# Kernel tuning notes

Hardware: AMD Instinct MI355X
Metric: run time of the kernel (lower is better)

Reference implementation:

```python
import jax, jax.numpy as jnp
import numpy as np

DIM = 128
N_ROUNDS = 120


def _mlp(x, W1, b1, W2, b2, W3, b3):
    h = jax.nn.relu(x @ W1.T + b1)
    h = jax.nn.relu(h @ W2.T + b2)
    return h @ W3.T + b3


def _lstm(x, h, c, Wih, Whh, bih, bhh):
    # torch nn.LSTM gate order: i, f, g, o
    g = x @ Wih.T + h @ Whh.T + (bih + bhh)
    i, f, gg, o = jnp.split(g, 4, axis=-1)
    c2 = jax.nn.sigmoid(f) * c + jax.nn.sigmoid(i) * jnp.tanh(gg)
    h2 = jax.nn.sigmoid(o) * jnp.tanh(c2)
    return h2, c2


def setup_inputs() -> dict:
    key = jax.random.key(0)
    keys = iter(jax.random.split(key, 64))
    def w(*shape):
        return jax.random.normal(next(keys), shape, dtype=jnp.float32) * 0.05
    n_nodes, n_vars = 8000, 1000
    N = n_nodes + n_vars
    # sparse 0/1 adjacency, stored dense as in the original (adj_matrix.values)
    adj = (jax.random.uniform(next(keys), (n_nodes, N)) < 0.003).astype(jnp.float32)
    values = jax.random.randint(next(keys), (N,), 0, 2)
    inp = dict(adj=adj, values=values, n_nodes=n_nodes)
    inp.update(true_W=w(DIM, 1), true_b=w(DIM), false_W=w(DIM, 1), false_b=w(DIM))
    for p in ("cm", "pm"):
        inp.update({p + "_W1": w(DIM, DIM), p + "_b1": w(DIM),
                    p + "_W2": w(DIM, DIM), p + "_b2": w(DIM),
                    p + "_W3": w(DIM, DIM), p + "_b3": w(DIM)})
    inp.update(vv_W1=w(DIM, DIM), vv_b1=w(DIM), vv_W2=w(DIM, DIM), vv_b2=w(DIM),
               vv_W3=w(1, DIM), vv_b3=w(1))
    for p in ("vu", "nu"):
        inp.update({p + "_Wih": w(4 * DIM, DIM), p + "_Whh": w(4 * DIM, DIM),
                    p + "_bih": w(4 * DIM), p + "_bhh": w(4 * DIM)})
    return inp


def reference(adj, values, n_nodes, true_W, true_b, false_W, false_b,
              cm_W1, cm_b1, cm_W2, cm_b2, cm_W3, cm_b3,
              pm_W1, pm_b1, pm_W2, pm_b2, pm_W3, pm_b3,
              vv_W1, vv_b1, vv_W2, vv_b2, vv_W3, vv_b3,
              vu_Wih, vu_Whh, vu_bih, vu_bhh,
              nu_Wih, nu_Whh, nu_bih, nu_bhh):
    init_ts = jnp.ones((1,), jnp.float32)
    true_vec = true_W @ init_ts + true_b     # (128,)
    false_vec = false_W @ init_ts + false_b  # (128,)
    h0 = jnp.where((values == 1)[:, None], true_vec, false_vec)  # (N,128)
    c0 = jnp.zeros_like(h0)

    def step(carry, _):
        h, c = carry
        var_pre = _mlp(h, cm_W1, cm_b1, cm_W2, cm_b2, cm_W3, cm_b3)   # (N,128)
        c2p = adj @ var_pre                                           # (n_nodes,128)
        hn, cn = _lstm(c2p, h[:n_nodes], c[:n_nodes], vu_Wih, vu_Whh, vu_bih, vu_bhh)
        h = jnp.concatenate([hn, h[n_nodes:]], axis=0)
        c = jnp.concatenate([cn, c[n_nodes:]], axis=0)
        node_pre = _mlp(h[:n_nodes], pm_W1, pm_b1, pm_W2, pm_b2, pm_W3, pm_b3)
        p2c = adj.T @ node_pre                                        # (N,128)
        h, c = _lstm(p2c, h, c, nu_Wih, nu_Whh, nu_bih, nu_bhh)
        return (h, c), None

    (h, c), _ = jax.lax.scan(step, (h0, c0), None, length=N_ROUNDS)
    vote = _mlp(h[n_nodes:], vv_W1, vv_b1, vv_W2, vv_b2, vv_W3, vv_b3)  # (n_vars,1)
    return vote.squeeze(-1)
```

## Files before the change

### kernel.cpp

```cpp
#include <hip/hip_runtime.h>
#include <cstddef>
#include <cstdint>

#define DIM 128
#define NROUNDS 120
#define NNZ_CAP (1 << 20)
#define NB 250
#define IDXCAP 3584
#define RING 6

typedef _Float16 half8 __attribute__((ext_vector_type(8)));
typedef float f32x4 __attribute__((ext_vector_type(4)));
typedef unsigned long long u64;

__device__ __forceinline__ float sigf(float x) { return 1.f / (1.f + __expf(-x)); }
__device__ __forceinline__ float tanh_fast(float x) { return 2.f / (1.f + __expf(-2.f * x)) - 1.f; }

__device__ __forceinline__ void st_bypass(_Float16* p, _Float16 v) {
  union { _Float16 f; unsigned short s; } u;
  u.f = v;
  __hip_atomic_store((unsigned short*)p, u.s, __ATOMIC_RELAXED, __HIP_MEMORY_SCOPE_AGENT);
}

__global__ void count_nz_kernel(const float* __restrict__ adj, int* __restrict__ row_cnt,
                                int* __restrict__ col_cnt, int ncols) {
  int i = blockIdx.x;
  int t4 = blockIdx.y * blockDim.x + threadIdx.x;
  int j0 = t4 * 4;
  int c = 0;
  if (j0 < ncols) {
    if ((ncols & 3) == 0) {
      float4 v = *(const float4*)(adj + (size_t)i * ncols + j0);
      if (v.x != 0.f) { atomicAdd(&col_cnt[j0 + 0], 1); ++c; }
      if (v.y != 0.f) { atomicAdd(&col_cnt[j0 + 1], 1); ++c; }
      if (v.z != 0.f) { atomicAdd(&col_cnt[j0 + 2], 1); ++c; }
      if (v.w != 0.f) { atomicAdd(&col_cnt[j0 + 3], 1); ++c; }
    } else {
      for (int e = 0; e < 4 && j0 + e < ncols; ++e)
        if (adj[(size_t)i * ncols + j0 + e] != 0.f) { atomicAdd(&col_cnt[j0 + e], 1); ++c; }
    }
  }
  for (int off = 32; off; off >>= 1) c += __shfl_down(c, off, 64);
  if ((threadIdx.x & 63) == 0 && c) atomicAdd(&row_cnt[i], c);
}

__global__ void scan_kernel(const int* __restrict__ cnt, int* __restrict__ ptr, int n) {
  __shared__ int sdata[256];
  int t = threadIdx.x;
  int per = (n + 255) / 256;
  int beg = t * per;
  int end = beg + per; if (end > n) end = n;
  int local = 0;
  for (int i = beg; i < end; ++i) local += cnt[i];
  sdata[t] = local;
  __syncthreads();
  for (int off = 1; off < 256; off <<= 1) {
    int v = (t >= off) ? sdata[t - off] : 0;
    __syncthreads();
    sdata[t] += v;
    __syncthreads();
  }
  int run = sdata[t] - local;
  for (int i = beg; i < end; ++i) { ptr[i] = run; run += cnt[i]; }
  if (t == 255) ptr[n] = sdata[255];
}

__global__ void copy_int_kernel(const int* __restrict__ a, int* __restrict__ b, int n) {
  int i = blockIdx.x * 256 + threadIdx.x;
  if (i < n) b[i] = a[i];
}

__global__ __launch_bounds__(64) void fill_csr_csc_kernel(const float* __restrict__ adj,
                                                          const int* __restrict__ row_ptr,
                                                          int* __restrict__ col_idx,
                                                          int* __restrict__ col_cur,
                                                          int* __restrict__ row_idx, int ncols) {
  int row = blockIdx.x;
  int lane = threadIdx.x;
  int base = row_ptr[row];
  int cursor = 0;
  const float* arow = adj + (size_t)row * ncols;
  for (int j0 = 0; j0 < ncols; j0 += 64) {
    int j = j0 + lane;
    bool nz = (j < ncols) && (arow[j] != 0.f);
    u64 m = __ballot(nz);
    int pre = __popcll(m & ((1ull << lane) - 1));
    if (nz) {
      col_idx[base + cursor + pre] = j;
      int t = atomicAdd(&col_cur[j], 1);
      row_idx[t] = row;
    }
    cursor += __popcll(m);
  }
}

__global__ void pack_w_kernel(const float* __restrict__ src, int out_dim,
                              _Float16* __restrict__ dh) {
  int idx = blockIdx.x * 256 + threadIdx.x;
  if (idx >= out_dim * DIM) return;
  int n = idx >> 7, k = idx & 127;
  _Float16 hi = (_Float16)src[idx];
  int nt = n >> 4, ks = k >> 5;
  int L = ((k >> 3) & 3) * 16 + (n & 15);
  int j = k & 7;
  dh[((nt * 4 + ks) * 64 + L) * 8 + j] = hi;
}

__global__ void pack_bias_kernel(const float* __restrict__ a, const float* __restrict__ b,
                                 float* __restrict__ o, int n) {
  int i = blockIdx.x * 256 + threadIdx.x;
  if (i < n) o[i] = a[i] + b[i];
}

__device__ __forceinline__ int sw_idx(int m, int k) {
  return (m << 7) + (((((k >> 3) ^ (m & 15))) << 3) | (k & 7));
}

__device__ __forceinline__ float touch(const _Float16* __restrict__ w, int n, int tid) {
  float t = 0.f;
  for (int i = tid * 64; i < n; i += 512 * 64) t += (float)w[i];
  return t;
}

template <int NS>
__device__ __forceinline__ void gather_lds(const int* Sidx, const int* lofs, const int* lcnt,
                                           int mbase,
                                           const int* __restrict__ gptr,
                                           const int* __restrict__ gidx,
                                           const _Float16* __restrict__ va, int rowlim,
                                           int b, int nb, _Float16* Xh, _Float16* Xl, int tid) {
  int seg = tid & 15;
  const char* vab = (const char*)va + seg * 16;
  for (int r = tid >> 4; r < NS * 16; r += 32) {
    float a[8];
#pragma unroll
    for (int e = 0; e < 8; ++e) a[e] = 0.f;
    int lo = lofs[mbase + r], c = lcnt[mbase + r];
    if (lo >= 0) {
      const int* ip = Sidx + lo;
      int p = 0;
      for (; p + 8 <= c; p += 8) {
        half8 v0 = *(const half8*)(vab + ip[p]);
        half8 v1 = *(const half8*)(vab + ip[p + 1]);
        half8 v2 = *(const half8*)(vab + ip[p + 2]);
        half8 v3 = *(const half8*)(vab + ip[p + 3]);
        half8 v4 = *(const half8*)(vab + ip[p + 4]);
        half8 v5 = *(const half8*)(vab + ip[p + 5]);
        half8 v6 = *(const half8*)(vab + ip[p + 6]);
        half8 v7 = *(const half8*)(vab + ip[p + 7]);
#pragma unroll
        for (int e = 0; e < 8; ++e)
          a[e] += (((float)v0[e] + (float)v1[e]) + ((float)v2[e] + (float)v3[e])) +
                  (((float)v4[e] + (float)v5[e]) + ((float)v6[e] + (float)v7[e]));
      }
      for (; p + 2 <= c; p += 2) {
        half8 v0 = *(const half8*)(vab + ip[p]);
        half8 v1 = *(const half8*)(vab + ip[p + 1]);
#pragma unroll
        for (int e = 0; e < 8; ++e) a[e] += (float)v0[e] + (float)v1[e];
      }
      if (p < c) {
        half8 v = *(const half8*)(vab + ip[p]);
#pragma unroll
        for (int e = 0; e < 8; ++e) a[e] += (float)v[e];
      }
    } else {
      int row = b + r * nb;
      if (row < rowlim) {
        int s0 = gptr[row], e_ = gptr[row + 1];
        for (int p = s0; p < e_; ++p) {
          half8 v = *(const half8*)(va + (size_t)gidx[p] * DIM + seg * 8);
#pragma unroll
          for (int e = 0; e < 8; ++e) a[e] += (float)v[e];
        }
      }
    }
    int aoff = sw_idx(r, seg * 8);
#pragma unroll
    for (int e = 0; e < 8; ++e) {
      _Float16 hi = (_Float16)a[e];
      Xh[aoff + e] = hi;
      Xl[aoff + e] = (_Float16)(a[e] - (float)hi);
    }
  }
}

__device__ __forceinline__ void mfma2(f32x4& acc, half8 ah, half8 al, half8 bh) {
  acc = __builtin_amdgcn_mfma_f32_16x16x32_f16(ah, bh, acc, 0, 0, 0);
  acc = __builtin_amdgcn_mfma_f32_16x16x32_f16(al, bh, acc, 0, 0, 0);
}

template <int NS>
__device__ __forceinline__ void mlp_layer_t(const _Float16* Ah_, const _Float16* Al_,
                                            const _Float16* __restrict__ Wh,
                                            const float* __restrict__ B,
                                            _Float16* Dh, _Float16* Dl, int tid) {
  int lane = tid & 63, w = tid >> 6;
  int m16 = lane & 15, quad = lane >> 4;
  float bv = B[w * 16 + m16];
  f32x4 acc[NS];
#pragma unroll
  for (int s = 0; s < NS; ++s) acc[s] = (f32x4){bv, bv, bv, bv};
#pragma unroll
  for (int ks = 0; ks < 4; ++ks) {
    int boff = ((w * 4 + ks) * 64 + lane) * 8;
    half8 bh = *(const half8*)(Wh + boff);
#pragma unroll
    for (int s = 0; s < NS; ++s) {
      int a_off = sw_idx(s * 16 + m16, ks * 32 + quad * 8);
      mfma2(acc[s], *(const half8*)(Ah_ + a_off), *(const half8*)(Al_ + a_off), bh);
    }
  }
#pragma unroll
  for (int s = 0; s < NS; ++s)
#pragma unroll
    for (int reg = 0; reg < 4; ++reg) {
      int rl = s * 16 + quad * 4 + reg;
      int col = w * 16 + m16;
      float x = fmaxf(acc[s][reg], 0.f);
      _Float16 hi = (_Float16)x;
      int a = sw_idx(rl, col);
      Dh[a] = hi;
      Dl[a] = (_Float16)(x - (float)hi);
    }
  __syncthreads();
}

template <int NS>
__device__ __forceinline__ void mlp_pers(const _Float16* Ah, const _Float16* Al,
                                         _Float16* T1h, _Float16* T1l,
                                         _Float16* T2h, _Float16* T2l,
                                         const _Float16* __restrict__ W1h, const float* __restrict__ b1,
                                         const _Float16* __restrict__ W2h, const float* __restrict__ b2,
                                         const _Float16* __restrict__ W3h, const float* __restrict__ b3,
                                         _Float16* __restrict__ out, int rowlim, int b, int nb,
                                         int tid) {
  mlp_layer_t<NS>(Ah, Al, W1h, b1, T1h, T1l, tid);
  mlp_layer_t<NS>(T1h, T1l, W2h, b2, T2h, T2l, tid);
  int lane = tid & 63, w = tid >> 6;
  int m16 = lane & 15, quad = lane >> 4;
  float bv = b3[w * 16 + m16];
  f32x4 acc[NS];
#pragma unroll
  for (int s = 0; s < NS; ++s) acc[s] = (f32x4){bv, bv, bv, bv};
#pragma unroll
  for (int ks = 0; ks < 4; ++ks) {
    int boff = ((w * 4 + ks) * 64 + lane) * 8;
    half8 bh = *(const half8*)(W3h + boff);
#pragma unroll
    for (int s = 0; s < NS; ++s) {
      int a_off = sw_idx(s * 16 + m16, ks * 32 + quad * 8);
      mfma2(acc[s], *(const half8*)(T2h + a_off), *(const half8*)(T2l + a_off), bh);
    }
  }
#pragma unroll
  for (int s = 0; s < NS; ++s)
#pragma unroll
    for (int reg = 0; reg < 4; ++reg) {
      int rl = s * 16 + quad * 4 + reg;
      int row = b + rl * nb;
      int col = w * 16 + m16;
      if (row < rowlim) st_bypass(out + (size_t)row * DIM + col, (_Float16)acc[s][reg]);
    }
}

template <int NS>
__device__ __forceinline__ void lstm_pers(const _Float16* Hh, const _Float16* Hl,
                                          const _Float16* Xh, const _Float16* Xl,
                                          const _Float16* __restrict__ Wxh,
                                          const _Float16* __restrict__ Whh_,
                                          const float* __restrict__ bcomb, int tid,
                                          f32x4 (&acc)[NS][4]) {
  int lane = tid & 63, w = tid >> 6;
  int m16 = lane & 15, quad = lane >> 4;
#pragma unroll
  for (int g = 0; g < 4; ++g) {
    float bv = bcomb[g * 128 + w * 16 + m16];
#pragma unroll
    for (int s = 0; s < NS; ++s) acc[s][g] = (f32x4){bv, bv, bv, bv};
  }
#pragma unroll
  for (int ks = 0; ks < 4; ++ks) {
    half8 ah[NS], al[NS];
#pragma unroll
    for (int s = 0; s < NS; ++s) {
      int a_off = sw_idx(s * 16 + m16, ks * 32 + quad * 8);
      ah[s] = *(const half8*)(Hh + a_off);
      al[s] = *(const half8*)(Hl + a_off);
    }
#pragma unroll
    for (int g = 0; g < 4; ++g) {
      int boff = (((g * 8 + w) * 4 + ks) * 64 + lane) * 8;
      half8 bh = *(const half8*)(Whh_ + boff);
#pragma unroll
      for (int s = 0; s < NS; ++s) mfma2(acc[s][g], ah[s], al[s], bh);
    }
#pragma unroll
    for (int s = 0; s < NS; ++s) {
      int a_off = sw_idx(s * 16 + m16, ks * 32 + quad * 8);
      ah[s] = *(const half8*)(Xh + a_off);
      al[s] = *(const half8*)(Xl + a_off);
    }
#pragma unroll
    for (int g = 0; g < 4; ++g) {
      int boff = (((g * 8 + w) * 4 + ks) * 64 + lane) * 8;
      half8 bh = *(const half8*)(Wxh + boff);
#pragma unroll
      for (int s = 0; s < NS; ++s) mfma2(acc[s][g], ah[s], al[s], bh);
    }
  }
}

#define GO_IDX (NB * 16)
__device__ __forceinline__ void gbar(unsigned* __restrict__ bar, int nblocks, unsigned ep,
                                     int b, int tid) {
  asm volatile("s_waitcnt vmcnt(0)" ::: "memory");
  __syncthreads();
  if (b == 0) {
    if (tid < 64) {
      int guard = 0;
      for (;;) {
        int ok = 1;
        for (int s = 1 + tid; s < nblocks; s += 64) {
          unsigned v = __hip_atomic_load(&bar[s * 16], __ATOMIC_RELAXED, __HIP_MEMORY_SCOPE_AGENT);
          ok &= (int)(v >= ep);
        }
        if (__all(ok)) break;
        __builtin_amdgcn_s_sleep(2);
        if (++guard > (1 << 15)) break;
      }
      if (tid == 0)
        __hip_atomic_store(&bar[GO_IDX], ep, __ATOMIC_RELAXED, __HIP_MEMORY_SCOPE_AGENT);
    }
  } else if (tid == 0) {
    __hip_atomic_store(&bar[b * 16], ep, __ATOMIC_RELAXED, __HIP_MEMORY_SCOPE_AGENT);
    int guard = 0;
    while (__hip_atomic_load(&bar[GO_IDX], __ATOMIC_RELAXED, __HIP_MEMORY_SCOPE_AGENT) < ep) {
      __builtin_amdgcn_s_sleep(8);
      if (++guard > (1 << 17)) break;
    }
  }
  __syncthreads();
}

#define SZ128 (DIM * DIM)
#define SZ512 (4 * DIM * DIM)
#define O_CM1 0
#define O_CM2 (SZ128)
#define O_CM3 (2 * SZ128)
#define O_PM1 (3 * SZ128)
#define O_PM2 (4 * SZ128)
#define O_PM3 (5 * SZ128)
#define O_VUX ((size_t)6 * SZ128)
#define O_VUH ((size_t)6 * SZ128 + SZ512)
#define O_NUX ((size_t)6 * SZ128 + 2 * SZ512)
#define O_NUH ((size_t)6 * SZ128 + 3 * SZ512)

#define LSLOT (3 * 2048 + 768)

template <int NS1>
__global__ __launch_bounds__(512, 2) void persist_kernel(
    const int* __restrict__ row_ptr, const int* __restrict__ col_idx,
    const int* __restrict__ col_ptr, const int* __restrict__ row_idx,
    const int* __restrict__ values, const float* __restrict__ tW, const float* __restrict__ tb,
    const float* __restrict__ fW, const float* __restrict__ fb,
    const _Float16* __restrict__ packh,
    const float* __restrict__ vu_b, const float* __restrict__ nu_b,
    const float* __restrict__ cm_b1, const float* __restrict__ cm_b2,
    const float* __restrict__ cm_b3, const float* __restrict__ pm_b1,
    const float* __restrict__ pm_b2, const float* __restrict__ pm_b3,
    _Float16* __restrict__ va1, _Float16* __restrict__ va2, size_t vstride,
    float* __restrict__ hout, unsigned* __restrict__ bar,
    int n_nodes, int N, int nblocks) {
  __shared__ _Float16 Hh[LSLOT], Hl[LSLOT], Xh[LSLOT], Xl[LSLOT], T2h[LSLOT], T2l[LSLOT];
  __shared__ int Sidx[IDXCAP];
  __shared__ int lofs[96], lcnt[96], gstb[96];
  int tid = threadIdx.x, b = blockIdx.x;
  int lane = tid & 63, w = tid >> 6, m16 = lane & 15, quad = lane >> 4;

  const _Float16* CM1 = packh + O_CM1;
  const _Float16* CM2 = packh + O_CM2;
  const _Float16* CM3 = packh + O_CM3;
  const _Float16* PM1 = packh + O_PM1;
  const _Float16* PM2 = packh + O_PM2;
  const _Float16* PM3 = packh + O_PM3;
  const _Float16* VUX = packh + O_VUX;
  const _Float16* VUH = packh + O_VUH;
  const _Float16* NUX = packh + O_NUX;
  const _Float16* NUH = packh + O_NUH;

  float cold[3][4];
#pragma unroll
  for (int s = 0; s < 3; ++s)
#pragma unroll
    for (int reg = 0; reg < 4; ++reg) {
      cold[s][reg] = 0.f;
      int rl = s * 16 + quad * 4 + reg;
      int row = b + rl * nblocks;
      int col = w * 16 + m16;
      float hv = 0.f;
      if (row < N) hv = (values[row] == 1) ? (tW[col] + tb[col]) : (fW[col] + fb[col]);
      int a = sw_idx(rl, col);
      _Float16 hi = (_Float16)hv;
      Hh[a] = hi;
      Hl[a] = (_Float16)(hv - (float)hi);
    }

  if (tid < 96) {
    int s = tid, row, c = 0, gs = 0;
    if (s < 48) {
      row = b + s * nblocks;
      if (row < n_nodes) { gs = row_ptr[row]; c = row_ptr[row + 1] - gs; }
    } else {
      row = b + (s - 48) * nblocks;
      if (row < N) { gs = col_ptr[row]; c = col_ptr[row + 1] - gs; }
    }
    gstb[s] = gs;
    lcnt[s] = c;
  }
  __syncthreads();
  if (tid == 0) {
    int cur = 0;
    for (int s = 0; s < 96; ++s) {
      int c = lcnt[s];
      if (c > 0 && cur + c <= IDXCAP) { lofs[s] = cur; cur += c; }
      else if (c > 0) lofs[s] = -1;
      else lofs[s] = 0;
    }
  }
  __syncthreads();
  for (int s = 0; s < 96; ++s) {
    int c = lcnt[s], lo = lofs[s];
    if (lo < 0 || c == 0) continue;
    int gs = gstb[s];
    const int* src = (s < 48) ? col_idx : row_idx;
    for (int i = tid; i < c; i += 512) Sidx[lo + i] = src[gs + i] << 8;
  }
  __syncthreads();

  unsigned ep = 0;
  {
    float tpf = touch(CM1, DIM * DIM, tid) + touch(CM2, DIM * DIM, tid) +
                touch(CM3, DIM * DIM, tid);
    asm volatile("" :: "v"(tpf));
  }
  mlp_pers<3>(Hh, Hl, Xh, Xl, T2h, T2l, CM1, cm_b1, CM2, cm_b2, CM3, cm_b3,
              va1, N, b, nblocks, tid);
  gbar(bar, nblocks, ++ep, b, tid);

  for (int r = 0; r < NROUNDS; ++r) {
    const _Float16* va1r = va1 + (size_t)(r % RING) * vstride;
    _Float16* va2w = va2 + (size_t)(r % RING) * vstride;
    _Float16* va1w = va1 + (size_t)((r + 1) % RING) * vstride;

    {
      gather_lds<NS1>(Sidx, lofs, lcnt, 0, row_ptr, col_idx, va1r, n_nodes, b, nblocks,
                      Xh, Xl, tid);
      float tpf = touch(VUX, 4 * DIM * DIM, tid) + touch(VUH, 4 * DIM * DIM, tid) +
                  touch(PM1, DIM * DIM, tid) + touch(PM2, DIM * DIM, tid) +
                  touch(PM3, DIM * DIM, tid);
      asm volatile("" :: "v"(tpf));
    }
    __syncthreads();
    {
      f32x4 acc[NS1][4];
      lstm_pers<NS1>(Hh, Hl, Xh, Xl, VUX, VUH, vu_b, tid, acc);
      __syncthreads();
#pragma unroll
      for (int s = 0; s < NS1; ++s)
#pragma unroll
        for (int reg = 0; reg < 4; ++reg) {
          int rl = s * 16 + quad * 4 + reg;
          int row = b + rl * nblocks;
          if (row < n_nodes) {
            float iv = sigf(acc[s][0][reg]);
            float fv = sigf(acc[s][1][reg]);
            float gv = tanh_fast(acc[s][2][reg]);
            float ov = sigf(acc[s][3][reg]);
            float cn = fv * cold[s][reg] + iv * gv;
            cold[s][reg] = cn;
            float hn = ov * tanh_fast(cn);
            int a = sw_idx(rl, w * 16 + m16);
            _Float16 hi = (_Float16)hn;
            Hh[a] = hi;
            Hl[a] = (_Float16)(hn - (float)hi);
          }
        }
    }
    __syncthreads();
    mlp_pers<NS1>(Hh, Hl, Xh, Xl, T2h, T2l, PM1, pm_b1, PM2, pm_b2, PM3, pm_b3,
                  va2w, n_nodes, b, nblocks, tid);
    gbar(bar, nblocks, ++ep, b, tid);

    bool last = (r == NROUNDS - 1);
    {
      gather_lds<3>(Sidx, lofs, lcnt, 48, col_ptr, row_idx, va2w, N, b, nblocks, Xh, Xl, tid);
      float tpf = touch(NUX, 4 * DIM * DIM, tid) + touch(NUH, 4 * DIM * DIM, tid) +
                  touch(CM1, DIM * DIM, tid) + touch(CM2, DIM * DIM, tid) +
                  touch(CM3, DIM * DIM, tid);
      asm volatile("" :: "v"(tpf));
    }
    __syncthreads();
    {
      f32x4 acc[3][4];
      lstm_pers<3>(Hh, Hl, Xh, Xl, NUX, NUH, nu_b, tid, acc);
      __syncthreads();
#pragma unroll
      for (int s = 0; s < 3; ++s)
#pragma unroll
        for (int reg = 0; reg < 4; ++reg) {
          int rl = s * 16 + quad * 4 + reg;
          int row = b + rl * nblocks;
          if (row < N) {
            float iv = sigf(acc[s][0][reg]);
            float fv = sigf(acc[s][1][reg]);
            float gv = tanh_fast(acc[s][2][reg]);
            float ov = sigf(acc[s][3][reg]);
            float cn = fv * cold[s][reg] + iv * gv;
            cold[s][reg] = cn;
            float hn = ov * tanh_fast(cn);
            if (last) {
              hout[(size_t)row * DIM + (w * 16 + m16)] = hn;
            } else {
              int a = sw_idx(rl, w * 16 + m16);
              _Float16 hi = (_Float16)hn;
              Hh[a] = hi;
              Hl[a] = (_Float16)(hn - (float)hi);
            }
          }
        }
    }
    if (!last) {
      __syncthreads();
      mlp_pers<3>(Hh, Hl, Xh, Xl, T2h, T2l, CM1, cm_b1, CM2, cm_b2, CM3, cm_b3,
                  va1w, N, b, nblocks, tid);
      gbar(bar, nblocks, ++ep, b, tid);
    }
  }
}

__device__ __forceinline__ void tile_gemm(const float* S, const float* __restrict__ W,
                                          int colB, int rowB, float acc[4][4]) {
#pragma unroll 4
  for (int kc = 0; kc < DIM; kc += 4) {
    float4 xv[4], wv[4];
#pragma unroll
    for (int r = 0; r < 4; ++r) xv[r] = *(const float4*)(S + (rowB + r) * DIM + kc);
#pragma unroll
    for (int c = 0; c < 4; ++c) wv[c] = *(const float4*)(W + (size_t)(colB + c) * DIM + kc);
#pragma unroll
    for (int r = 0; r < 4; ++r)
#pragma unroll
      for (int c = 0; c < 4; ++c)
        acc[r][c] += xv[r].x * wv[c].x + xv[r].y * wv[c].y + xv[r].z * wv[c].z + xv[r].w * wv[c].w;
  }
}

__device__ __forceinline__ void layer_lds(const float* Sin, float* Sout,
                                          const float* __restrict__ W, const float* __restrict__ B,
                                          bool relu, int colB, int rowB) {
  float acc[4][4];
#pragma unroll
  for (int r = 0; r < 4; ++r)
#pragma unroll
    for (int cc = 0; cc < 4; ++cc) acc[r][cc] = B[colB + cc];
  tile_gemm(Sin, W, colB, rowB, acc);
#pragma unroll
  for (int r = 0; r < 4; ++r) {
    float4 v;
    v.x = acc[r][0]; v.y = acc[r][1]; v.z = acc[r][2]; v.w = acc[r][3];
    if (relu) { v.x = fmaxf(v.x, 0.f); v.y = fmaxf(v.y, 0.f); v.z = fmaxf(v.z, 0.f); v.w = fmaxf(v.w, 0.f); }
    *(float4*)&Sout[(rowB + r) * DIM + colB] = v;
  }
  __syncthreads();
}

__global__ __launch_bounds__(256) void vote_kernel(
    const float* __restrict__ X, int M,
    const float* __restrict__ W1, const float* __restrict__ b1,
    const float* __restrict__ W2, const float* __restrict__ b2,
    const float* __restrict__ W3, const float* __restrict__ b3,
    float* __restrict__ out) {
  __shared__ float Xs[32 * DIM];
  __shared__ float Ys[32 * DIM];
  int tid = threadIdx.x;
  int rb = blockIdx.x * 32;
  int mrows = M - rb; if (mrows > 32) mrows = 32;
  {
    const float4* src = (const float4*)(X + (size_t)rb * DIM);
    float4* dst = (float4*)Xs;
    int nf4 = mrows * (DIM / 4);
    for (int t = tid; t < 32 * (DIM / 4); t += 256) {
      float4 v;
      if (t < nf4) v = src[t];
      else { v.x = v.y = v.z = v.w = 0.f; }
      dst[t] = v;
    }
  }
  __syncthreads();
  int tx = tid & 31, ty = tid >> 5;
  int colB = tx * 4, rowB = ty * 4;
  layer_lds(Xs, Ys, W1, b1, true, colB, rowB);
  layer_lds(Ys, Xs, W2, b2, true, colB, rowB);
  if (tid < 32) {
    int gr = rb + tid;
    if (gr < M) {
      float s = b3[0];
      for (int k = 0; k < DIM; ++k) s += Xs[tid * DIM + k] * W3[k];
      out[gr] = s;
    }
  }
}

extern "C" void kernel_launch(void* const* d_in, const int* in_sizes, int n_in,
                              void* d_out, int out_size, void* d_ws, size_t ws_size,
                              hipStream_t stream) {
  const float* adj    = (const float*)d_in[0];
  const int*   values = (const int*)d_in[1];
  const int N       = in_sizes[1];
  const int n_nodes = in_sizes[0] / N;
  const int n_vars  = N - n_nodes;

  const float* true_W  = (const float*)d_in[3];
  const float* true_b  = (const float*)d_in[4];
  const float* false_W = (const float*)d_in[5];
  const float* false_b = (const float*)d_in[6];
  const float* cm_W1 = (const float*)d_in[7];
  const float* cm_b1 = (const float*)d_in[8];
  const float* cm_W2 = (const float*)d_in[9];
  const float* cm_b2 = (const float*)d_in[10];
  const float* cm_W3 = (const float*)d_in[11];
  const float* cm_b3 = (const float*)d_in[12];
  const float* pm_W1 = (const float*)d_in[13];
  const float* pm_b1 = (const float*)d_in[14];
  const float* pm_W2 = (const float*)d_in[15];
  const float* pm_b2 = (const float*)d_in[16];
  const float* pm_W3 = (const float*)d_in[17];
  const float* pm_b3 = (const float*)d_in[18];
  const float* vv_W1 = (const float*)d_in[19];
  const float* vv_b1 = (const float*)d_in[20];
  const float* vv_W2 = (const float*)d_in[21];
  const float* vv_b2 = (const float*)d_in[22];
  const float* vv_W3 = (const float*)d_in[23];
  const float* vv_b3 = (const float*)d_in[24];
  const float* vu_Wih = (const float*)d_in[25];
  const float* vu_Whh = (const float*)d_in[26];
  const float* vu_bih = (const float*)d_in[27];
  const float* vu_bhh = (const float*)d_in[28];
  const float* nu_Wih = (const float*)d_in[29];
  const float* nu_Whh = (const float*)d_in[30];
  const float* nu_bih = (const float*)d_in[31];
  const float* nu_bhh = (const float*)d_in[32];

  uintptr_t p = (uintptr_t)d_ws;
  auto take = [&](size_t bytes) -> void* {
    uintptr_t cur = (p + 255) & ~(uintptr_t)255;
    p = cur + bytes;
    return (void*)cur;
  };
  size_t vs = (size_t)N * DIM;
  float* h   = (float*)take((size_t)N * DIM * sizeof(float));
  _Float16* va1 = (_Float16*)take(vs * RING * sizeof(_Float16));
  _Float16* va2 = (_Float16*)take(vs * RING * sizeof(_Float16));
  int* row_ptr = (int*)take((size_t)(n_nodes + 1) * sizeof(int));
  int* col_ptr = (int*)take((size_t)(N + 1) * sizeof(int));
  int* cnts    = (int*)take((size_t)(n_nodes + N) * sizeof(int));
  int* row_cnt = cnts;
  int* col_cnt = cnts + n_nodes;
  int* col_cur = (int*)take((size_t)N * sizeof(int));
  int* col_idx = (int*)take((size_t)NNZ_CAP * sizeof(int));
  int* row_idx = (int*)take((size_t)NNZ_CAP * sizeof(int));

  size_t tot_pack = (size_t)6 * SZ128 + (size_t)4 * SZ512;
  _Float16* packh = (_Float16*)take(tot_pack * sizeof(_Float16));
  float* vu_b = (float*)take(512 * sizeof(float));
  float* nu_b = (float*)take(512 * sizeof(float));
  unsigned* bar = (unsigned*)take((size_t)(NB + 2) * 16 * sizeof(unsigned));

  hipMemsetAsync(cnts, 0, (size_t)(n_nodes + N) * sizeof(int), stream);
  hipMemsetAsync(bar, 0, (size_t)(NB + 2) * 16 * sizeof(unsigned), stream);

  int cols4 = (N + 3) / 4;
  dim3 cgrid(n_nodes, (cols4 + 255) / 256);
  count_nz_kernel<<<cgrid, 256, 0, stream>>>(adj, row_cnt, col_cnt, N);
  scan_kernel<<<1, 256, 0, stream>>>(row_cnt, row_ptr, n_nodes);
  scan_kernel<<<1, 256, 0, stream>>>(col_cnt, col_ptr, N);
  copy_int_kernel<<<(N + 255) / 256, 256, 0, stream>>>(col_ptr, col_cur, N);
  fill_csr_csc_kernel<<<n_nodes, 64, 0, stream>>>(adj, row_ptr, col_idx, col_cur, row_idx, N);

  auto pack = [&](const float* src, int out_dim, size_t o) {
    pack_w_kernel<<<(out_dim * DIM + 255) / 256, 256, 0, stream>>>(src, out_dim, packh + o);
  };
  pack(cm_W1, DIM, O_CM1); pack(cm_W2, DIM, O_CM2); pack(cm_W3, DIM, O_CM3);
  pack(pm_W1, DIM, O_PM1); pack(pm_W2, DIM, O_PM2); pack(pm_W3, DIM, O_PM3);
  pack(vu_Wih, 4 * DIM, O_VUX); pack(vu_Whh, 4 * DIM, O_VUH);
  pack(nu_Wih, 4 * DIM, O_NUX); pack(nu_Whh, 4 * DIM, O_NUH);
  pack_bias_kernel<<<2, 256, 0, stream>>>(vu_bih, vu_bhh, vu_b, 512);
  pack_bias_kernel<<<2, 256, 0, stream>>>(nu_bih, nu_bhh, nu_b, 512);

  int ns1 = (n_nodes + NB * 16 - 1) / (NB * 16);
  if (ns1 <= 2) {
    persist_kernel<2><<<NB, 512, 0, stream>>>(
        row_ptr, col_idx, col_ptr, row_idx, values, true_W, true_b, false_W, false_b,
        packh, vu_b, nu_b, cm_b1, cm_b2, cm_b3, pm_b1, pm_b2, pm_b3,
        va1, va2, vs, h, bar, n_nodes, N, NB);
  } else {
    persist_kernel<3><<<NB, 512, 0, stream>>>(
        row_ptr, col_idx, col_ptr, row_idx, values, true_W, true_b, false_W, false_b,
        packh, vu_b, nu_b, cm_b1, cm_b2, cm_b3, pm_b1, pm_b2, pm_b3,
        va1, va2, vs, h, bar, n_nodes, N, NB);
  }

  vote_kernel<<<(n_vars + 31) / 32, 256, 0, stream>>>(h + (size_t)n_nodes * DIM, n_vars,
      vv_W1, vv_b1, vv_W2, vv_b2, vv_W3, vv_b3, (float*)d_out);
}
```

Baseline: 10.31 ms.

## Stage MLP output through LDS for 16-byte stores and prewarm gathered activations

The final MLP layer now writes its fp16 results into an LDS tile first. After a block barrier, each row is written to global memory as 16-byte vector stores with sc0/sc1 cache bits, replacing per-element atomic 2-byte stores. Before each gather, every block also touches a slice of the activation buffer it is about to read, partitioned across blocks, to bring it into cache ahead of the random gather. This trades an extra LDS round-trip, a barrier and extra prefetch loads for fewer, wider global transactions and lower gather latency.

```diff
diff --git a/kernel.cpp b/kernel.cpp
--- a/kernel.cpp
+++ b/kernel.cpp
@@ -16,10 +16,8 @@
 __device__ __forceinline__ float sigf(float x) { return 1.f / (1.f + __expf(-x)); }
 __device__ __forceinline__ float tanh_fast(float x) { return 2.f / (1.f + __expf(-2.f * x)) - 1.f; }
 
-__device__ __forceinline__ void st_bypass(_Float16* p, _Float16 v) {
-  union { _Float16 f; unsigned short s; } u;
-  u.f = v;
-  __hip_atomic_store((unsigned short*)p, u.s, __ATOMIC_RELAXED, __HIP_MEMORY_SCOPE_AGENT);
+__device__ __forceinline__ void st16(void* a, half8 v) {
+  asm volatile("global_store_dwordx4 %0, %1, off sc0 sc1" :: "v"(a), "v"(v) : "memory");
 }
 
 __global__ void count_nz_kernel(const float* __restrict__ adj, int* __restrict__ row_cnt,
@@ -122,6 +120,17 @@
   return t;
 }
 
+__device__ __forceinline__ float warm_va(const _Float16* __restrict__ v, size_t elems,
+                                         int b, int nblocks, int tid) {
+  int res = b & 7;
+  int nsl = (nblocks - 1 - res) / 8 + 1;
+  int sl = b >> 3;
+  size_t beg = elems * (size_t)sl / nsl, end = elems * (size_t)(sl + 1) / nsl;
+  float t = 0.f;
+  for (size_t i = beg + (size_t)tid * 32; i < end; i += 512 * 32) t += (float)v[i];
+  return t;
+}
+
 template <int NS>
 __device__ __forceinline__ void gather_lds(const int* Sidx, const int* lofs, const int* lcnt,
                                            int mbase,
@@ -258,10 +267,19 @@
 #pragma unroll
     for (int reg = 0; reg < 4; ++reg) {
       int rl = s * 16 + quad * 4 + reg;
-      int row = b + rl * nb;
-      int col = w * 16 + m16;
-      if (row < rowlim) st_bypass(out + (size_t)row * DIM + col, (_Float16)acc[s][reg]);
-    }
+      T1h[rl * DIM + w * 16 + m16] = (_Float16)acc[s][reg];
+    }
+  __syncthreads();
+  {
+    int seg = tid & 15;
+    for (int r = tid >> 4; r < NS * 16; r += 32) {
+      int row = b + r * nb;
+      if (row < rowlim) {
+        half8 v = *(const half8*)(T1h + r * DIM + seg * 8);
+        st16(out + (size_t)row * DIM + seg * 8, v);
+      }
+    }
+  }
 }
 
 template <int NS>
@@ -454,11 +472,12 @@
     _Float16* va1w = va1 + (size_t)((r + 1) % RING) * vstride;
 
     {
+      float tpf = warm_va(va1r, (size_t)N * DIM, b, nblocks, tid);
       gather_lds<NS1>(Sidx, lofs, lcnt, 0, row_ptr, col_idx, va1r, n_nodes, b, nblocks,
                       Xh, Xl, tid);
-      float tpf = touch(VUX, 4 * DIM * DIM, tid) + touch(VUH, 4 * DIM * DIM, tid) +
-                  touch(PM1, DIM * DIM, tid) + touch(PM2, DIM * DIM, tid) +
-                  touch(PM3, DIM * DIM, tid);
+      tpf += touch(VUX, 4 * DIM * DIM, tid) + touch(VUH, 4 * DIM * DIM, tid) +
+             touch(PM1, DIM * DIM, tid) + touch(PM2, DIM * DIM, tid) +
+             touch(PM3, DIM * DIM, tid);
       asm volatile("" :: "v"(tpf));
     }
     __syncthreads();
@@ -494,10 +513,11 @@
 
     bool last = (r == NROUNDS - 1);
     {
+      float tpf = warm_va(va2w, (size_t)n_nodes * DIM, b, nblocks, tid);
       gather_lds<3>(Sidx, lofs, lcnt, 48, col_ptr, row_idx, va2w, N, b, nblocks, Xh, Xl, tid);
-      float tpf = touch(NUX, 4 * DIM * DIM, tid) + touch(NUH, 4 * DIM * DIM, tid) +
-                  touch(CM1, DIM * DIM, tid) + touch(CM2, DIM * DIM, tid) +
-                  touch(CM3, DIM * DIM, tid);
+      tpf += touch(NUX, 4 * DIM * DIM, tid) + touch(NUH, 4 * DIM * DIM, tid) +
+             touch(CM1, DIM * DIM, tid) + touch(CM2, DIM * DIM, tid) +
+             touch(CM3, DIM * DIM, tid);
       asm volatile("" :: "v"(tpf));
     }
     __syncthreads();
```

New measurement: 10.21 ms. No clear change (-1.0%).
